# Performance work log

Measured on AMD Instinct MI355X. Metric: run time of the kernel, lower is better.

Reference implementation:

```python
import jax, jax.numpy as jnp
import numpy as np

B, S, DM, H = 16, 512, 256, 8
DF = DM // H          # per-head feature dim
K_INDEX = 5           # keep top-(K_INDEX) probs per row (SparseKT soft-threshold top-k)
NEG_MASK = -1e32      # fill for causal mask
NEG_SPARSE = -1e16    # fill for sub-threshold probs before re-softmax


def setup_inputs() -> dict:
    key = jax.random.key(0)
    ks = jax.random.split(key, 6)
    sc = 1.0 / np.sqrt(DM)  # ~xavier scale
    q = jax.random.normal(ks[0], (B, S, DM), jnp.float32)
    k = jax.random.normal(ks[1], (B, S, DM), jnp.float32)
    v = jax.random.normal(ks[2], (B, S, DM), jnp.float32)
    # causal lower-triangular mask, [1,1,S,S]; scores where mask==0 -> -1e32
    mask = jnp.tril(jnp.ones((S, S), jnp.int32))[None, None]
    # k_linear / v_linear / out_proj weights (key_query_same=True -> q shares k_linear)
    Wk = jax.random.normal(ks[3], (DM, DM), jnp.float32) * sc
    Wv = jax.random.normal(ks[4], (DM, DM), jnp.float32) * sc
    Wo = jax.random.normal(ks[5], (DM, DM), jnp.float32) * sc
    bk = jnp.zeros((DM,), jnp.float32)
    bv = jnp.zeros((DM,), jnp.float32)
    bo = jnp.zeros((DM,), jnp.float32)
    return {"q": q, "k": k, "v": v, "mask": mask, "zero_pad": 1,
            "Wk": Wk, "bk": bk, "Wv": Wv, "bv": bv, "Wo": Wo, "bo": bo}


def _heads(x, W, b):
    # Linear then split heads: [B,S,DM] -> [B,H,S,DF]
    y = x @ W.T + b
    return y.reshape(B, S, H, DF).transpose(0, 2, 1, 3)


def reference(q, k, v, mask, zero_pad, Wk, bk, Wv, bv, Wo, bo):
    qh = _heads(q, Wk, bk)  # key_query_same: q uses k_linear
    kh = _heads(k, Wk, bk)
    vh = _heads(v, Wv, bv)

    scores = jnp.einsum("bhqd,bhkd->bhqk", qh, kh) / np.sqrt(DF)
    scores = jnp.where(mask == 0, jnp.float32(NEG_MASK), scores)
    attn = jax.nn.softmax(scores, axis=-1)

    if K_INDEX + 1 < S:
        attn_a = attn[:, :, : K_INDEX + 1, :]          # short rows kept as-is
        attn_b = attn[:, :, K_INDEX + 1 :, :]          # rows to sparsify
        # threshold = K_INDEX-th largest prob per row (== sorted desc [k_index-1])
        thr = jax.lax.top_k(attn_b, K_INDEX)[0][..., -1:]
        attn_b = jnp.where(attn_b - thr >= 0, attn_b, jnp.float32(NEG_SPARSE))
        attn_b = jax.nn.softmax(attn_b, axis=-1)
        attn = jnp.concatenate([attn_a, attn_b], axis=2)

    if zero_pad:
        attn = jnp.concatenate(
            [jnp.zeros_like(attn[:, :, :1, :]), attn[:, :, 1:, :]], axis=2)

    # dropout is identity in eval mode
    ctx = jnp.einsum("bhqk,bhkd->bhqd", attn, vh)
    concat = ctx.transpose(0, 2, 1, 3).reshape(B, S, DM)
    output = concat @ Wo.T + bo
    return output, attn
```

## Files before the change

### kernel.cpp

```cpp
#include <hip/hip_runtime.h>
#include <hip/hip_bf16.h>
#include <math.h>

#define BB 16
#define SS 512
#define DMM 256
#define HH 8
#define DFF 32
#define KIDX 5

template<int TM, int TN, int GM, int GN, bool HEADS>
__device__ __forceinline__ void gemm_body(
    const float* __restrict__ X, const float* __restrict__ W,
    const float* __restrict__ bias, float* __restrict__ Y)
{
  __shared__ float As[16][TM];
  __shared__ float Bs[16][TN];
  constexpr int NA = TM / 64;
  constexpr int NB = TN / 64;
  const int tid = threadIdx.x;
  const int tx = tid & 15;
  const int ty = tid >> 4;
  const int m0 = blockIdx.x * TM;
  const int n0 = blockIdx.y * TN;

  float4 pa[NA], pb[NB];
  #pragma unroll
  for (int i = 0; i < NA; ++i) {
    const int f = tid * NA + i;
    pa[i] = *reinterpret_cast<const float4*>(&X[(size_t)(m0 + (f >> 2)) * DMM + ((f & 3) << 2)]);
  }
  #pragma unroll
  for (int i = 0; i < NB; ++i) {
    const int f = tid * NB + i;
    pb[i] = *reinterpret_cast<const float4*>(&W[(size_t)(n0 + (f >> 2)) * DMM + ((f & 3) << 2)]);
  }

  float acc[GM * 4][GN * 4] = {};

  for (int k0 = 0; k0 < DMM; k0 += 16) {
    #pragma unroll
    for (int i = 0; i < NA; ++i) {
      const int f = tid * NA + i;
      const int r = f >> 2, c4 = (f & 3) << 2;
      As[c4 + 0][r] = pa[i].x; As[c4 + 1][r] = pa[i].y;
      As[c4 + 2][r] = pa[i].z; As[c4 + 3][r] = pa[i].w;
    }
    #pragma unroll
    for (int i = 0; i < NB; ++i) {
      const int f = tid * NB + i;
      const int r = f >> 2, c4 = (f & 3) << 2;
      Bs[c4 + 0][r] = pb[i].x; Bs[c4 + 1][r] = pb[i].y;
      Bs[c4 + 2][r] = pb[i].z; Bs[c4 + 3][r] = pb[i].w;
    }
    __syncthreads();
    if (k0 + 16 < DMM) {
      #pragma unroll
      for (int i = 0; i < NA; ++i) {
        const int f = tid * NA + i;
        pa[i] = *reinterpret_cast<const float4*>(&X[(size_t)(m0 + (f >> 2)) * DMM + k0 + 16 + ((f & 3) << 2)]);
      }
      #pragma unroll
      for (int i = 0; i < NB; ++i) {
        const int f = tid * NB + i;
        pb[i] = *reinterpret_cast<const float4*>(&W[(size_t)(n0 + (f >> 2)) * DMM + k0 + 16 + ((f & 3) << 2)]);
      }
    }
    #pragma unroll
    for (int kk = 0; kk < 16; ++kk) {
      float4 af[GM], bf[GN];
      #pragma unroll
      for (int gm = 0; gm < GM; ++gm)
        af[gm] = *reinterpret_cast<const float4*>(&As[kk][gm * (TM / 2) + ty * 4]);
      #pragma unroll
      for (int gn = 0; gn < GN; ++gn)
        bf[gn] = *reinterpret_cast<const float4*>(&Bs[kk][gn * (TN / 2) + tx * 4]);
      #pragma unroll
      for (int gm = 0; gm < GM; ++gm) {
        const float am[4] = {af[gm].x, af[gm].y, af[gm].z, af[gm].w};
        #pragma unroll
        for (int i = 0; i < 4; ++i) {
          #pragma unroll
          for (int gn = 0; gn < GN; ++gn) {
            acc[gm*4+i][gn*4+0] = fmaf(am[i], bf[gn].x, acc[gm*4+i][gn*4+0]);
            acc[gm*4+i][gn*4+1] = fmaf(am[i], bf[gn].y, acc[gm*4+i][gn*4+1]);
            acc[gm*4+i][gn*4+2] = fmaf(am[i], bf[gn].z, acc[gm*4+i][gn*4+2]);
            acc[gm*4+i][gn*4+3] = fmaf(am[i], bf[gn].w, acc[gm*4+i][gn*4+3]);
          }
        }
      }
    }
    __syncthreads();
  }

  #pragma unroll
  for (int gn = 0; gn < GN; ++gn) {
    const int n = n0 + gn * (TN / 2) + tx * 4;
    const float4 b4 = *reinterpret_cast<const float4*>(&bias[n]);
    #pragma unroll
    for (int gm = 0; gm < GM; ++gm) {
      #pragma unroll
      for (int i = 0; i < 4; ++i) {
        const int m = m0 + gm * (TM / 2) + ty * 4 + i;
        float4 o;
        o.x = acc[gm*4+i][gn*4+0] + b4.x;
        o.y = acc[gm*4+i][gn*4+1] + b4.y;
        o.z = acc[gm*4+i][gn*4+2] + b4.z;
        o.w = acc[gm*4+i][gn*4+3] + b4.w;
        if (HEADS) {
          const int bb = m >> 9;
          const int s  = m & (SS - 1);
          const int hh = n >> 5;
          const int d  = n & (DFF - 1);
          *reinterpret_cast<float4*>(&Y[(((size_t)bb * HH + hh) * SS + s) * DFF + d]) = o;
        } else {
          *reinterpret_cast<float4*>(&Y[(size_t)m * DMM + n]) = o;
        }
      }
    }
  }
}

__global__ __launch_bounds__(256) void proj_kernel(
    const float* __restrict__ q, const float* __restrict__ k, const float* __restrict__ v,
    const float* __restrict__ Wk, const float* __restrict__ bk,
    const float* __restrict__ Wv, const float* __restrict__ bv,
    float* __restrict__ qh, float* __restrict__ kh, float* __restrict__ vh)
{
  const int z = blockIdx.z;
  const float* X = (z == 0) ? q : (z == 1) ? k : v;
  const float* W = (z == 2) ? Wv : Wk;
  const float* bias = (z == 2) ? bv : bk;
  float* Y = (z == 0) ? qh : (z == 1) ? kh : vh;
  gemm_body<128, 128, 2, 2, true>(X, W, bias, Y);
}

__global__ __launch_bounds__(256) void out_kernel(
    const float* __restrict__ X, const float* __restrict__ Wo,
    const float* __restrict__ bo, float* __restrict__ Y)
{
  gemm_body<128, 64, 2, 1, false>(X, Wo, bo, Y);
}

__device__ __forceinline__ void attn_row_tail(
    float* p, const int qrow, const int lane,
    const int b, const int h, const int bh,
    const int* __restrict__ zp,
    float* __restrict__ attn, float* __restrict__ concat,
    const float* __restrict__ vb,
    float* wsw, int* wsc)
{
  const int ncols = qrow + 1;

  float m = p[0];
  #pragma unroll
  for (int s2 = 1; s2 < 8; ++s2) m = fmaxf(m, p[s2]);
  #pragma unroll
  for (int off = 32; off >= 1; off >>= 1) m = fmaxf(m, __shfl_xor(m, off, 64));
  float sum = 0.f;
  #pragma unroll
  for (int s2 = 0; s2 < 8; ++s2) {
    const float e = (p[s2] == -INFINITY) ? 0.f : __expf(p[s2] - m);
    p[s2] = e;
    sum += e;
  }
  #pragma unroll
  for (int off = 32; off >= 1; off >>= 1) sum += __shfl_xor(sum, off, 64);
  const float inv = 1.0f / sum;
  #pragma unroll
  for (int s2 = 0; s2 < 8; ++s2) p[s2] *= inv;

  float neww[8];
  if (qrow > KIDX) {
    float v[8];
    #pragma unroll
    for (int s2 = 0; s2 < 8; ++s2) {
      const int col = lane + (s2 << 6);
      v[s2] = (col < ncols) ? p[s2] : -INFINITY;
    }
    #define CE(i, j) { const float t = fmaxf(v[i], v[j]); v[j] = fminf(v[i], v[j]); v[i] = t; }
    CE(0,1) CE(2,3) CE(4,5) CE(6,7)
    CE(0,2) CE(1,3) CE(4,6) CE(5,7)
    CE(1,2) CE(5,6)
    CE(0,4) CE(1,5) CE(2,6) CE(3,7)
    CE(2,4) CE(3,5)
    CE(1,2) CE(3,4) CE(5,6)
    #undef CE
    float a0 = v[0], a1 = v[1], a2 = v[2], a3 = v[3], a4 = v[4];
    #pragma unroll
    for (int off = 1; off <= 32; off <<= 1) {
      const float b0 = __shfl_xor(a0, off, 64);
      const float b1 = __shfl_xor(a1, off, 64);
      const float b2 = __shfl_xor(a2, off, 64);
      const float b3 = __shfl_xor(a3, off, 64);
      const float b4 = __shfl_xor(a4, off, 64);
      const float n0 = fmaxf(a0, b0);
      const float n1 = fmaxf(fmaxf(a1, b1), fminf(a0, b0));
      const float n2 = fmaxf(fmaxf(a2, b2), fmaxf(fminf(a0, b1), fminf(a1, b0)));
      const float n3 = fmaxf(fmaxf(a3, b3),
                       fmaxf(fmaxf(fminf(a0, b2), fminf(a1, b1)), fminf(a2, b0)));
      const float n4 = fmaxf(fmaxf(a4, b4),
                       fmaxf(fmaxf(fminf(a0, b3), fminf(a1, b2)),
                             fmaxf(fminf(a2, b1), fminf(a3, b0))));
      a0 = n0; a1 = n1; a2 = n2; a3 = n3; a4 = n4;
    }
    const float m1 = a0;
    const float thr = a4;
    float nsum = 0.f;
    #pragma unroll
    for (int s2 = 0; s2 < 8; ++s2) {
      const int col = lane + (s2 << 6);
      float e = 0.f;
      if (col < ncols && (p[s2] - thr >= 0.f)) e = __expf(p[s2] - m1);
      neww[s2] = e;
      nsum += e;
    }
    #pragma unroll
    for (int off = 32; off >= 1; off >>= 1) nsum += __shfl_xor(nsum, off, 64);
    const float ninv = 1.0f / nsum;
    #pragma unroll
    for (int s2 = 0; s2 < 8; ++s2) neww[s2] *= ninv;
  } else {
    #pragma unroll
    for (int s2 = 0; s2 < 8; ++s2) neww[s2] = p[s2];
  }

  if (qrow == 0 && *zp != 0) {
    #pragma unroll
    for (int s2 = 0; s2 < 8; ++s2) neww[s2] = 0.f;
  }

  {
    float* arow = attn + ((size_t)bh * SS + qrow) * SS;
    #pragma unroll
    for (int s2 = 0; s2 < 8; ++s2) arow[lane + (s2 << 6)] = neww[s2];
  }

  {
    unsigned long long msks[8];
    #pragma unroll
    for (int s2 = 0; s2 < 8; ++s2) msks[s2] = __ballot(neww[s2] != 0.f);
    int rbase = 0;
    #pragma unroll
    for (int s2 = 0; s2 < 8; ++s2) {
      const unsigned long long msk = msks[s2];
      const int myr = rbase + __popcll(msk & ((1ull << lane) - 1ull));
      if (((msk >> lane) & 1ull) && myr < 8) {
        wsw[myr] = neww[s2];
        wsc[myr] = (s2 << 6) | lane;
      }
      rbase += __popcll(msk);
    }
    const int nk = rbase;
    if (lane < 8 && lane >= nk) { wsw[lane] = 0.f; wsc[lane] = 0; }

    const int dd = lane & 31;
    float accv = 0.f;
    if (nk <= 8) {
      #pragma unroll
      for (int i = 0; i < 8; ++i)
        accv += wsw[i] * vb[(size_t)wsc[i] * DFF + dd];
    } else {
      #pragma unroll
      for (int s2 = 0; s2 < 8; ++s2) {
        unsigned long long msk = msks[s2];
        while (msk) {
          const int src = __ffsll(msk) - 1;
          msk &= msk - 1;
          accv += __shfl(neww[s2], src, 64) * vb[(size_t)(src + (s2 << 6)) * DFF + dd];
        }
      }
    }
    if (lane < 32)
      concat[((size_t)b * SS + qrow) * DMM + h * DFF + dd] = accv;
  }
}

__global__ __launch_bounds__(256) void attn_kernel(
    const float* __restrict__ qh,
    const float* __restrict__ kh,
    const float* __restrict__ vh,
    const int* __restrict__ zp,
    float* __restrict__ attn,
    float* __restrict__ concat)
{
  __shared__ float4 Ksh[64 * 8];
  __shared__ float ws_w[4][8];
  __shared__ int   ws_c[4][8];

  const int tid  = threadIdx.x;
  const int lane = tid & 63;
  const int wave = tid >> 6;
  const int grp  = blockIdx.x;
  const int bh   = grp >> 6;
  const int base = (grp & 63) << 3;
  const int rA   = base + wave;
  const int rB   = rA + 4;
  const int b    = bh >> 3;
  const int h    = bh & 7;
  const float scale = 0.17677669529663688f;

  const float* kb = kh + (size_t)bh * SS * DFF;
  const float* vb = vh + (size_t)bh * SS * DFF;

  float4 qA[8], qB[8];
  {
    const float* qpA = qh + ((size_t)bh * SS + rA) * DFF;
    const float* qpB = qh + ((size_t)bh * SS + rB) * DFF;
    #pragma unroll
    for (int g = 0; g < 8; ++g) {
      qA[g] = *reinterpret_cast<const float4*>(qpA + g * 4);
      qB[g] = *reinterpret_cast<const float4*>(qpB + g * 4);
    }
  }

  const int nch = (base >> 6) + 1;

  const int scol = tid & 63;
  const int g0   = (tid >> 6) << 1;

  float pA[8], pB[8];
  #pragma unroll
  for (int i = 0; i < 8; ++i) { pA[i] = -INFINITY; pB[i] = -INFINITY; }

  const float* kp0 = kb + (size_t)scol * DFF + g0 * 4;
  float4 r0 = *reinterpret_cast<const float4*>(kp0);
  float4 r1 = *reinterpret_cast<const float4*>(kp0 + 4);

  for (int c = 0; c < nch; ++c) {
    Ksh[(scol << 3) + ((g0 + scol) & 7)]     = r0;
    Ksh[(scol << 3) + ((g0 + 1 + scol) & 7)] = r1;
    __syncthreads();
    if (c + 1 < nch) {
      const float* kp = kb + (size_t)(((c + 1) << 6) + scol) * DFF + g0 * 4;
      r0 = *reinterpret_cast<const float4*>(kp);
      r1 = *reinterpret_cast<const float4*>(kp + 4);
    }
    {
      const int col = (c << 6) + lane;
      float d0A = 0.f, d1A = 0.f, d0B = 0.f, d1B = 0.f;
      #pragma unroll
      for (int g = 0; g < 8; ++g) {
        const float4 kv = Ksh[(lane << 3) + ((g + lane) & 7)];
        const float4 qa = qA[g];
        const float4 qb = qB[g];
        d0A = fmaf(qa.x, kv.x, d0A);
        d1A = fmaf(qa.y, kv.y, d1A);
        d0A = fmaf(qa.z, kv.z, d0A);
        d1A = fmaf(qa.w, kv.w, d1A);
        d0B = fmaf(qb.x, kv.x, d0B);
        d1B = fmaf(qb.y, kv.y, d1B);
        d0B = fmaf(qb.z, kv.z, d0B);
        d1B = fmaf(qb.w, kv.w, d1B);
      }
      if (col <= rA) pA[c] = (d0A + d1A) * scale;
      if (col <= rB) pB[c] = (d0B + d1B) * scale;
    }
    __syncthreads();
  }

  attn_row_tail(pA, rA, lane, b, h, bh, zp, attn, concat, vb, ws_w[wave], ws_c[wave]);
  attn_row_tail(pB, rB, lane, b, h, bh, zp, attn, concat, vb, ws_w[wave], ws_c[wave]);
}

extern "C" void kernel_launch(void* const* d_in, const int* in_sizes, int n_in,
                              void* d_out, int out_size, void* d_ws, size_t ws_size,
                              hipStream_t stream) {
  const float* q  = (const float*)d_in[0];
  const float* k  = (const float*)d_in[1];
  const float* v  = (const float*)d_in[2];
  const int*   zp = (const int*)d_in[4];
  const float* Wk = (const float*)d_in[5];
  const float* bk = (const float*)d_in[6];
  const float* Wv = (const float*)d_in[7];
  const float* bv = (const float*)d_in[8];
  const float* Wo = (const float*)d_in[9];
  const float* bo = (const float*)d_in[10];

  float* ws     = (float*)d_ws;
  float* qhp    = ws;
  float* khp    = ws + 2097152;
  float* vhp    = ws + 4194304;
  float* concat = ws + 6291456;

  float* outp  = (float*)d_out;
  float* attnp = outp + (size_t)BB * SS * DMM;

  proj_kernel<<<dim3(64, 2, 3), 256, 0, stream>>>(q, k, v, Wk, bk, Wv, bv, qhp, khp, vhp);
  attn_kernel<<<dim3(BB * HH * SS / 8), 256, 0, stream>>>(qhp, khp, vhp, zp, attnp, concat);
  out_kernel<<<dim3(64, 4), 256, 0, stream>>>(concat, Wo, bo, outp);
}
```

Baseline: 324.9 us.

## Zero-fill attn separately, write only nonzero probs, reorder blocks, double-buffer K

A dedicated fill kernel zeroes the full attention output up front. The attention kernel then stores only the nonzero probabilities, or just the valid columns for the short rows, so the scattered writes shrink. Blocks are remapped so the longest causal rows are scheduled first, and the K-tile loop is unrolled by two with two register prefetch buffers. The output GEMM switches to smaller 64x64 tiles with twice the blocks. The cost is an extra full-size memset pass and more launches, in exchange for fewer scattered stores and better load balance.

```diff
diff --git a/kernel.cpp b/kernel.cpp
--- a/kernel.cpp
+++ b/kernel.cpp
@@ -121,6 +121,16 @@
   }
 }
 
+__global__ __launch_bounds__(256) void fill_kernel(float* __restrict__ attnp)
+{
+  float4* dst = reinterpret_cast<float4*>(attnp);
+  const float4 zero = {0.f, 0.f, 0.f, 0.f};
+  const size_t total = (size_t)BB * HH * SS * SS / 4;
+  for (size_t i = (size_t)blockIdx.x * 256 + threadIdx.x; i < total;
+       i += (size_t)gridDim.x * 256)
+    dst[i] = zero;
+}
+
 __global__ __launch_bounds__(256) void proj_kernel(
     const float* __restrict__ q, const float* __restrict__ k, const float* __restrict__ v,
     const float* __restrict__ Wk, const float* __restrict__ bk,
@@ -139,7 +149,7 @@
     const float* __restrict__ X, const float* __restrict__ Wo,
     const float* __restrict__ bo, float* __restrict__ Y)
 {
-  gemm_body<128, 64, 2, 1, false>(X, Wo, bo, Y);
+  gemm_body<64, 64, 1, 1, false>(X, Wo, bo, Y);
 }
 
 __device__ __forceinline__ void attn_row_tail(
@@ -232,8 +242,13 @@
 
   {
     float* arow = attn + ((size_t)bh * SS + qrow) * SS;
-    #pragma unroll
-    for (int s2 = 0; s2 < 8; ++s2) arow[lane + (s2 << 6)] = neww[s2];
+    if (qrow <= KIDX) {
+      if (lane < ncols) arow[lane] = neww[0];
+    } else {
+      #pragma unroll
+      for (int s2 = 0; s2 < 8; ++s2)
+        if (neww[s2] != 0.f) arow[lane + (s2 << 6)] = neww[s2];
+    }
   }
 
   {
@@ -293,7 +308,7 @@
   const int wave = tid >> 6;
   const int grp  = blockIdx.x;
   const int bh   = grp >> 6;
-  const int base = (grp & 63) << 3;
+  const int base = ((grp & 63) ^ 63) << 3;
   const int rA   = base + wave;
   const int rB   = rA + 4;
   const int b    = bh >> 3;
@@ -323,41 +338,56 @@
   #pragma unroll
   for (int i = 0; i < 8; ++i) { pA[i] = -INFINITY; pB[i] = -INFINITY; }
 
-  const float* kp0 = kb + (size_t)scol * DFF + g0 * 4;
-  float4 r0 = *reinterpret_cast<const float4*>(kp0);
-  float4 r1 = *reinterpret_cast<const float4*>(kp0 + 4);
-
-  for (int c = 0; c < nch; ++c) {
-    Ksh[(scol << 3) + ((g0 + scol) & 7)]     = r0;
-    Ksh[(scol << 3) + ((g0 + 1 + scol) & 7)] = r1;
+#define LOADK(ra, rb_, cc) {                                                  \
+    const float* kp = kb + (size_t)(((cc) << 6) + scol) * DFF + g0 * 4;       \
+    ra  = *reinterpret_cast<const float4*>(kp);                               \
+    rb_ = *reinterpret_cast<const float4*>(kp + 4); }
+
+#define STAGEK(ra, rb_) {                                                     \
+    Ksh[(scol << 3) + ((g0 + scol) & 7)]     = ra;                            \
+    Ksh[(scol << 3) + ((g0 + 1 + scol) & 7)] = rb_; }
+
+#define COMPUTE(cc) {                                                         \
+    const int col = ((cc) << 6) + lane;                                       \
+    float d0A = 0.f, d1A = 0.f, d0B = 0.f, d1B = 0.f;                         \
+    _Pragma("unroll")                                                         \
+    for (int g = 0; g < 8; ++g) {                                             \
+      const float4 kv = Ksh[(lane << 3) + ((g + lane) & 7)];                  \
+      const float4 qa = qA[g];                                                \
+      const float4 qb = qB[g];                                                \
+      d0A = fmaf(qa.x, kv.x, d0A);                                            \
+      d1A = fmaf(qa.y, kv.y, d1A);                                            \
+      d0A = fmaf(qa.z, kv.z, d0A);                                            \
+      d1A = fmaf(qa.w, kv.w, d1A);                                            \
+      d0B = fmaf(qb.x, kv.x, d0B);                                            \
+      d1B = fmaf(qb.y, kv.y, d1B);                                            \
+      d0B = fmaf(qb.z, kv.z, d0B);                                            \
+      d1B = fmaf(qb.w, kv.w, d1B);                                            \
+    }                                                                         \
+    if (col <= rA) pA[(cc)] = (d0A + d1A) * scale;                            \
+    if (col <= rB) pB[(cc)] = (d0B + d1B) * scale; }
+
+  float4 a0, a1, b0 = {}, b1 = {};
+  LOADK(a0, a1, 0);
+  if (nch > 1) LOADK(b0, b1, 1);
+
+  for (int c = 0; c < nch; c += 2) {
+    STAGEK(a0, a1);
+    __syncthreads();
+    if (c + 2 < nch) LOADK(a0, a1, c + 2);
+    COMPUTE(c);
     __syncthreads();
     if (c + 1 < nch) {
-      const float* kp = kb + (size_t)(((c + 1) << 6) + scol) * DFF + g0 * 4;
-      r0 = *reinterpret_cast<const float4*>(kp);
-      r1 = *reinterpret_cast<const float4*>(kp + 4);
-    }
-    {
-      const int col = (c << 6) + lane;
-      float d0A = 0.f, d1A = 0.f, d0B = 0.f, d1B = 0.f;
-      #pragma unroll
-      for (int g = 0; g < 8; ++g) {
-        const float4 kv = Ksh[(lane << 3) + ((g + lane) & 7)];
-        const float4 qa = qA[g];
-        const float4 qb = qB[g];
-        d0A = fmaf(qa.x, kv.x, d0A);
-        d1A = fmaf(qa.y, kv.y, d1A);
-        d0A = fmaf(qa.z, kv.z, d0A);
-        d1A = fmaf(qa.w, kv.w, d1A);
-        d0B = fmaf(qb.x, kv.x, d0B);
-        d1B = fmaf(qb.y, kv.y, d1B);
-        d0B = fmaf(qb.z, kv.z, d0B);
-        d1B = fmaf(qb.w, kv.w, d1B);
-      }
-      if (col <= rA) pA[c] = (d0A + d1A) * scale;
-      if (col <= rB) pB[c] = (d0B + d1B) * scale;
-    }
-    __syncthreads();
-  }
+      STAGEK(b0, b1);
+      __syncthreads();
+      if (c + 3 < nch) LOADK(b0, b1, c + 3);
+      COMPUTE(c + 1);
+      __syncthreads();
+    }
+  }
+#undef LOADK
+#undef STAGEK
+#undef COMPUTE
 
   attn_row_tail(pA, rA, lane, b, h, bh, zp, attn, concat, vb, ws_w[wave], ws_c[wave]);
   attn_row_tail(pB, rB, lane, b, h, bh, zp, attn, concat, vb, ws_w[wave], ws_c[wave]);
@@ -386,7 +416,8 @@
   float* outp  = (float*)d_out;
   float* attnp = outp + (size_t)BB * SS * DMM;
 
+  fill_kernel<<<dim3(2048), 256, 0, stream>>>(attnp);
   proj_kernel<<<dim3(64, 2, 3), 256, 0, stream>>>(q, k, v, Wk, bk, Wv, bv, qhp, khp, vhp);
   attn_kernel<<<dim3(BB * HH * SS / 8), 256, 0, stream>>>(qhp, khp, vhp, zp, attnp, concat);
-  out_kernel<<<dim3(64, 4), 256, 0, stream>>>(concat, Wo, bo, outp);
-}
+  out_kernel<<<dim3(128, 4), 256, 0, stream>>>(concat, Wo, bo, outp);
+}
```

Measured after the change: 346.9 us. 1.07x slower.
